# Kernel optimization log

Measured on AMD Instinct MI355X. Metric: run time of the kernel, lower is better.

Reference implementation:

```python
import jax, jax.numpy as jnp
import numpy as np

NUM_NODES = 100000
NUM_EDGES = 2500000
NUM_GRAPHS = 512
NODE_DIM = 7
STATE_DIM = 32
M = 2
ROUNDS = 4


def setup_inputs() -> dict:
    key = jax.random.key(0)
    ks = jax.random.split(key, 16)
    x = jax.random.normal(ks[0], (NUM_NODES, NODE_DIM), dtype=jnp.float32)
    edge_index = jax.random.randint(ks[1], (2, NUM_EDGES), 0, NUM_NODES)
    batch = jnp.sort(jax.random.randint(ks[2], (NUM_NODES,), 0, NUM_GRAPHS))
    s = 1.0 / np.sqrt(STATE_DIM)
    W_in = jax.random.normal(ks[3], (NODE_DIM, STATE_DIM), dtype=jnp.float32) / np.sqrt(NODE_DIM)
    b_in = jnp.zeros((STATE_DIM,), dtype=jnp.float32)
    W_msg = jax.random.normal(ks[4], (ROUNDS, STATE_DIM, STATE_DIM), dtype=jnp.float32) * s
    b_msg = jnp.zeros((ROUNDS, STATE_DIM), dtype=jnp.float32)
    W_upd = jax.random.normal(ks[5], (ROUNDS, STATE_DIM, STATE_DIM), dtype=jnp.float32) * s
    b_upd = jnp.zeros((ROUNDS, STATE_DIM), dtype=jnp.float32)
    W_out = jax.random.normal(ks[6], (STATE_DIM, 2 * M), dtype=jnp.float32) * s
    b_out = jnp.zeros((2 * M,), dtype=jnp.float32)
    return {"x": x, "edge_index": edge_index, "batch": batch,
            "W_in": W_in, "b_in": b_in, "W_msg": W_msg, "b_msg": b_msg,
            "W_upd": W_upd, "b_upd": b_upd, "W_out": W_out, "b_out": b_out}


def reference(x, edge_index, batch, W_in, b_in, W_msg, b_msg, W_upd, b_upd, W_out, b_out):
    # input net
    state = jax.nn.relu(x @ W_in + b_in)  # (N, S)
    src, dst = edge_index[0], edge_index[1]
    for r in range(ROUNDS):
        message = jax.nn.relu(state @ W_msg[r] + b_msg[r])          # (N, S)
        gathered = message[src]                                      # (E, S) irregular gather
        aggregated = jax.ops.segment_sum(gathered, dst, num_segments=NUM_NODES)  # scatter-add
        state = state + jax.nn.relu(aggregated @ W_upd[r] + b_upd[r])
    graph_state = jax.ops.segment_sum(state, batch, num_segments=NUM_GRAPHS)     # (G, S)
    out = graph_state @ W_out + b_out                                # (G, 2M)
    mean, log_std = jnp.split(out, 2, axis=-1)
    # Gaussian head: return mean and std (scale = exp(log_std)) concatenated
    return jnp.concatenate([mean, jnp.exp(log_std)], axis=-1)
```

## Files before the change

### kernel.cpp

```cpp
#include <hip/hip_runtime.h>
#include <hip/hip_fp8.h>
#include <math.h>

#define N_NODES 100000
#define N_EDGES 2500000
#define N_GRAPHS 512
#define NODE_DIM 7
#define S 32
#define ROUNDS 4

#define BKT_SHIFT 8
#define BKT_NODES 256
#define NBKT ((N_NODES + BKT_NODES - 1) / BKT_NODES)
#define CAP 7168
#define NSLOT 64
#define SLOT_PAD 32
#define CUR_PAD 32

#define NBIN_BLOCKS 512
#define NBIN_THREADS 512
#define TILE ((N_EDGES + NBIN_BLOCKS - 1) / NBIN_BLOCKS)

#define GN (N_NODES * S / 256)
#define GG (N_NODES / 16)

__device__ __forceinline__ void block_max_publish(float v, float* slots, int bid, int tid) {
    __shared__ float wmax[4];
#pragma unroll
    for (int o = 32; o > 0; o >>= 1) v = fmaxf(v, __shfl_xor(v, o, 64));
    if ((tid & 63) == 0) wmax[tid >> 6] = v;
    __syncthreads();
    if (tid == 0) {
        float m = fmaxf(fmaxf(wmax[0], wmax[1]), fmaxf(wmax[2], wmax[3]));
        atomicMax((unsigned int*)&slots[(bid & (NSLOT - 1)) * SLOT_PAD], __float_as_uint(m));
    }
}

__device__ __forceinline__ void acc4_fp8(unsigned int u, float& a0, float& a1,
                                         float& a2, float& a3) {
#if __has_builtin(__builtin_amdgcn_cvt_pk_f32_fp8)
    typedef float v2f __attribute__((ext_vector_type(2)));
    v2f lo = __builtin_amdgcn_cvt_pk_f32_fp8((int)u, false);
    v2f hi = __builtin_amdgcn_cvt_pk_f32_fp8((int)u, true);
    a0 += lo.x; a1 += lo.y; a2 += hi.x; a3 += hi.y;
#else
    __hip_fp8_e4m3 t0, t1, t2, t3;
    t0.__x = u & 0xff; t1.__x = (u >> 8) & 0xff;
    t2.__x = (u >> 16) & 0xff; t3.__x = (u >> 24) & 0xff;
    a0 += (float)t0; a1 += (float)t1; a2 += (float)t2; a3 += (float)t3;
#endif
}

__global__ void k_input(const float* __restrict__ x, const float* __restrict__ W_in,
                        const float* __restrict__ b_in, float* __restrict__ state,
                        float* __restrict__ graph_state, int* __restrict__ cursor,
                        float* __restrict__ tmpmax) {
    __shared__ float sW[NODE_DIM * S];
    __shared__ float sb[S];
    __shared__ float wmax[4];
    int tid = threadIdx.x;
    if (tid < NODE_DIM * S) sW[tid] = W_in[tid];
    if (tid < S) sb[tid] = b_in[tid];
    __syncthreads();
    int gid = blockIdx.x * blockDim.x + tid;
    if (gid < N_GRAPHS * S) graph_state[gid] = 0.f;
    if (gid < NBKT * CUR_PAD) cursor[gid] = 0;
    int n = gid >> 5, j = gid & 31;
    float acc = sb[j];
#pragma unroll
    for (int k = 0; k < NODE_DIM; k++) acc += x[n * NODE_DIM + k] * sW[k * S + j];
    float v = fmaxf(acc, 0.f);
    state[gid] = v;
#pragma unroll
    for (int o = 32; o > 0; o >>= 1) v = fmaxf(v, __shfl_xor(v, o, 64));
    if ((tid & 63) == 0) wmax[tid >> 6] = v;
    __syncthreads();
    if (tid == 0)
        tmpmax[blockIdx.x] = fmaxf(fmaxf(wmax[0], wmax[1]), fmaxf(wmax[2], wmax[3]));
}

__global__ void k_bin(const int* __restrict__ src, const int* __restrict__ dst,
                      int* __restrict__ cursor, int* __restrict__ binned,
                      const float* __restrict__ tmpmax, float* __restrict__ smax0) {
    __shared__ int pval[TILE];
    __shared__ unsigned short bkt[TILE];
    __shared__ unsigned short sidx[TILE];
    __shared__ int cnt[NBKT];
    __shared__ int base[NBKT];
    __shared__ int gbase[NBKT];
    __shared__ int sm[NBIN_THREADS];
    __shared__ float red[8];
    int tid = threadIdx.x;
    if (blockIdx.x == 0) {
        float mx = 0.f;
        for (int i = tid; i < GN; i += NBIN_THREADS) mx = fmaxf(mx, tmpmax[i]);
#pragma unroll
        for (int o = 32; o > 0; o >>= 1) mx = fmaxf(mx, __shfl_xor(mx, o, 64));
        if ((tid & 63) == 0) red[tid >> 6] = mx;
        __syncthreads();
        if (tid == 0) {
            float g = 0.f;
#pragma unroll
            for (int k = 0; k < 8; k++) g = fmaxf(g, red[k]);
            smax0[0] = g;
        } else if (tid < NSLOT) {
            smax0[tid * SLOT_PAD] = 0.f;
        }
    }
    int b0 = blockIdx.x * TILE;
    int m = min(TILE, N_EDGES - b0);
    if (m < 0) m = 0;
    for (int k = tid; k < NBKT; k += NBIN_THREADS) cnt[k] = 0;
    __syncthreads();
    for (int i = tid; i < m; i += NBIN_THREADS) {
        int d = dst[b0 + i];
        int s = src[b0 + i];
        int k = d >> BKT_SHIFT;
        pval[i] = (s << BKT_SHIFT) | (d & (BKT_NODES - 1));
        bkt[i] = (unsigned short)k;
        atomicAdd(&cnt[k], 1);
    }
    __syncthreads();
    int v = (tid < NBKT) ? cnt[tid] : 0;
    sm[tid] = v;
    __syncthreads();
    for (int off = 1; off < NBIN_THREADS; off <<= 1) {
        int add = (tid >= off) ? sm[tid - off] : 0;
        __syncthreads();
        sm[tid] += add;
        __syncthreads();
    }
    if (tid < NBKT) {
        base[tid] = sm[tid] - v;
        gbase[tid] = v ? atomicAdd(&cursor[tid * CUR_PAD], v) : 0;
        cnt[tid] = 0;
    }
    __syncthreads();
    for (int i = tid; i < m; i += NBIN_THREADS) {
        int k = bkt[i];
        int r = atomicAdd(&cnt[k], 1);
        sidx[base[k] + r] = (unsigned short)i;
    }
    __syncthreads();
    for (int i = tid; i < m; i += NBIN_THREADS) {
        int e = sidx[i];
        int k = bkt[e];
        int lpos = gbase[k] + (i - base[k]);
        if (lpos < CAP)
            binned[(size_t)k * CAP + lpos] = pval[e];
    }
}

__global__ void k_fill2(const int* __restrict__ cursor, int* __restrict__ binned,
                        int* __restrict__ row_beg, int* __restrict__ row_end) {
    __shared__ int stage[CAP];
    __shared__ int cnt[BKT_NODES];
    __shared__ int sm[BKT_NODES];
    int tid = threadIdx.x;
    int bkt = blockIdx.x;
    int beg = bkt * CAP;
    int m = min(cursor[bkt * CUR_PAD], CAP);
    for (int i = tid; i < m; i += 256) stage[i] = binned[beg + i];
    cnt[tid] = 0;
    __syncthreads();
    for (int i = tid; i < m; i += 256) atomicAdd(&cnt[stage[i] & (BKT_NODES - 1)], 1);
    __syncthreads();
    int v = cnt[tid];
    sm[tid] = v;
    __syncthreads();
    for (int off = 1; off < BKT_NODES; off <<= 1) {
        int add = (tid >= off) ? sm[tid - off] : 0;
        __syncthreads();
        sm[tid] += add;
        __syncthreads();
    }
    {
        int excl = sm[tid] - v;
        cnt[tid] = excl;
        int n = bkt * BKT_NODES + tid;
        if (n < N_NODES) { row_beg[n] = beg + excl; row_end[n] = beg + excl + v; }
    }
    __syncthreads();
    for (int i = tid; i < m; i += 256) {
        int ent = stage[i];
        int p = atomicAdd(&cnt[ent & (BKT_NODES - 1)], 1);
        binned[beg + p] = ent >> BKT_SHIFT;
    }
}

__global__ void k_msg(const float* __restrict__ state, const float* __restrict__ W,
                      const float* __restrict__ b, const float* __restrict__ smax_slots,
                      float* __restrict__ smax_next, float* __restrict__ inv_scale_out,
                      __hip_fp8_e4m3* __restrict__ message) {
    __shared__ float sW[S * S];
    __shared__ float sb[S];
    __shared__ float ssc[S];
    int tid = threadIdx.x;
    if (blockIdx.x < NSLOT && tid == 0) smax_next[blockIdx.x * SLOT_PAD] = 0.f;
    for (int i = tid; i < S * S; i += 256) sW[i] = W[i];
    if (tid < S) sb[tid] = b[tid];
    __syncthreads();
    if (tid < S) {
        float smax = 0.f;
#pragma unroll
        for (int k = 0; k < NSLOT; k++) smax = fmaxf(smax, smax_slots[k * SLOT_PAD]);
        float cs = 0.f;
#pragma unroll
        for (int k = 0; k < S; k++) cs += fabsf(sW[k * S + tid]);
        float bound = smax * cs + fabsf(sb[tid]) + 1e-20f;
        int e = (int)floorf(log2f(400.f / bound));
        e = max(-60, min(60, e));
        ssc[tid] = exp2f((float)e);
        if (blockIdx.x == 0) inv_scale_out[tid] = exp2f((float)-e);
    }
    __syncthreads();
    int gid = blockIdx.x * 256 + tid;
    int j = tid & 31;
    float my = state[gid];
    float acc = sb[j];
#pragma unroll
    for (int k = 0; k < S; k++) acc += __shfl(my, k, 32) * sW[k * S + j];
    float m = fminf(fmaxf(acc, 0.f) * ssc[j], 440.f);
    message[gid] = __hip_fp8_e4m3(m);
}

__global__ void k_gather_upd(const int* __restrict__ row_beg, const int* __restrict__ row_end,
                             const int* __restrict__ csr_src,
                             const unsigned char* __restrict__ message,
                             const float* __restrict__ W, const float* __restrict__ b,
                             const float* __restrict__ inv_scale,
                             float* __restrict__ state, float* __restrict__ smax_next) {
    __shared__ float sW[S * S];
    __shared__ float sb[S];
    __shared__ float si[S];
    int tid = threadIdx.x;
    for (int i = tid; i < S * S; i += 256) sW[i] = W[i];
    if (tid < S) { sb[tid] = b[tid]; si[tid] = inv_scale[tid]; }
    __syncthreads();
    int g = tid >> 5, j = tid & 31;
    int n0 = blockIdx.x * 16 + g * 2;
    int n1 = n0 + 1;
    int es = j >> 3;
    int qd = j & 7;
    int b0 = row_beg[n0], e0 = row_end[n0];
    int b1 = row_beg[n1], e1 = row_end[n1];
    float a0 = 0.f, a1 = 0.f, a2 = 0.f, a3 = 0.f;
    float c0 = 0.f, c1 = 0.f, c2 = 0.f, c3 = 0.f;
    for (; b0 < e0 || b1 < e1; b0 += 32, b1 += 32) {
        int sid0 = (b0 + j < e0) ? csr_src[b0 + j] : 0;
        int sid1 = (b1 + j < e1) ? csr_src[b1 + j] : 0;
        unsigned int u0[8], u1[8];
#pragma unroll
        for (int p = 0; p < 8; p++) {
            int s = __shfl(sid0, p * 4 + es, 32);
            unsigned int* ap = (unsigned int*)(message + (unsigned)s * 32u + (unsigned)qd * 4u);
            u0[p] = __hip_atomic_load(ap, __ATOMIC_RELAXED, __HIP_MEMORY_SCOPE_AGENT);
        }
#pragma unroll
        for (int p = 0; p < 8; p++) {
            int s = __shfl(sid1, p * 4 + es, 32);
            unsigned int* ap = (unsigned int*)(message + (unsigned)s * 32u + (unsigned)qd * 4u);
            u1[p] = __hip_atomic_load(ap, __ATOMIC_RELAXED, __HIP_MEMORY_SCOPE_AGENT);
        }
#pragma unroll
        for (int p = 0; p < 8; p++) {
            unsigned int uv = (b0 + p * 4 + es < e0) ? u0[p] : 0u;
            acc4_fp8(uv, a0, a1, a2, a3);
        }
#pragma unroll
        for (int p = 0; p < 8; p++) {
            unsigned int uv = (b1 + p * 4 + es < e1) ? u1[p] : 0u;
            acc4_fp8(uv, c0, c1, c2, c3);
        }
    }
    a0 += __shfl_xor(a0, 8, 32); a0 += __shfl_xor(a0, 16, 32);
    a1 += __shfl_xor(a1, 8, 32); a1 += __shfl_xor(a1, 16, 32);
    a2 += __shfl_xor(a2, 8, 32); a2 += __shfl_xor(a2, 16, 32);
    a3 += __shfl_xor(a3, 8, 32); a3 += __shfl_xor(a3, 16, 32);
    c0 += __shfl_xor(c0, 8, 32); c0 += __shfl_xor(c0, 16, 32);
    c1 += __shfl_xor(c1, 8, 32); c1 += __shfl_xor(c1, 16, 32);
    c2 += __shfl_xor(c2, 8, 32); c2 += __shfl_xor(c2, 16, 32);
    c3 += __shfl_xor(c3, 8, 32); c3 += __shfl_xor(c3, 16, 32);
    float s0 = si[4 * qd + 0], s1 = si[4 * qd + 1];
    float s2 = si[4 * qd + 2], s3 = si[4 * qd + 3];
    a0 *= s0; a1 *= s1; a2 *= s2; a3 *= s3;
    c0 *= s0; c1 *= s1; c2 *= s2; c3 *= s3;
    float u0v = sb[j], u1v = sb[j];
#pragma unroll
    for (int k = 0; k < S; k++) {
        float av, cv;
        switch (k & 3) {
            case 0: av = __shfl(a0, k >> 2, 32); cv = __shfl(c0, k >> 2, 32); break;
            case 1: av = __shfl(a1, k >> 2, 32); cv = __shfl(c1, k >> 2, 32); break;
            case 2: av = __shfl(a2, k >> 2, 32); cv = __shfl(c2, k >> 2, 32); break;
            default: av = __shfl(a3, k >> 2, 32); cv = __shfl(c3, k >> 2, 32); break;
        }
        float w = sW[k * S + j];
        u0v += av * w;
        u1v += cv * w;
    }
    size_t i0 = (size_t)n0 * S + j, i1 = (size_t)n1 * S + j;
    float ns0 = state[i0] + fmaxf(u0v, 0.f);
    float ns1 = state[i1] + fmaxf(u1v, 0.f);
    state[i0] = ns0;
    state[i1] = ns1;
    block_max_publish(fmaxf(ns0, ns1), smax_next, blockIdx.x, tid);
}

__global__ void k_pool(const float* __restrict__ state, const int* __restrict__ batch,
                       float* __restrict__ graph_state) {
    const int CHUNK = 32;
    const int nchunks = (N_NODES + CHUNK - 1) / CHUNK;
    int gid = blockIdx.x * blockDim.x + threadIdx.x;
    if (gid >= nchunks * S) return;
    int c = gid >> 5, j = gid & 31;
    int n0 = c * CHUNK;
    int n1 = min(n0 + CHUNK, N_NODES);
    float acc = 0.f;
    int curb = batch[n0];
    for (int n = n0; n < n1; n++) {
        int bn = batch[n];
        if (bn != curb) {
            atomicAdd(&graph_state[curb * S + j], acc);
            acc = 0.f;
            curb = bn;
        }
        acc += state[(size_t)n * S + j];
    }
    atomicAdd(&graph_state[curb * S + j], acc);
}

__global__ void k_head(const float* __restrict__ graph_state, const float* __restrict__ W_out,
                       const float* __restrict__ b_out, float* __restrict__ out) {
    int gid = blockIdx.x * blockDim.x + threadIdx.x;
    if (gid >= N_GRAPHS * 4) return;
    int g = gid >> 2, j = gid & 3;
    float acc = b_out[j];
#pragma unroll
    for (int k = 0; k < S; k++) acc += graph_state[g * S + k] * W_out[k * 4 + j];
    out[gid] = (j < 2) ? acc : expf(fminf(acc, 88.0f));
}

extern "C" void kernel_launch(void* const* d_in, const int* in_sizes, int n_in,
                              void* d_out, int out_size, void* d_ws, size_t ws_size,
                              hipStream_t stream) {
    const float* x     = (const float*)d_in[0];
    const int*   ei    = (const int*)d_in[1];
    const int*   batch = (const int*)d_in[2];
    const float* W_in  = (const float*)d_in[3];
    const float* b_in  = (const float*)d_in[4];
    const float* W_msg = (const float*)d_in[5];
    const float* b_msg = (const float*)d_in[6];
    const float* W_upd = (const float*)d_in[7];
    const float* b_upd = (const float*)d_in[8];
    const float* W_out = (const float*)d_in[9];
    const float* b_out = (const float*)d_in[10];
    float* out = (float*)d_out;

    float* state            = (float*)d_ws;
    __hip_fp8_e4m3* message = (__hip_fp8_e4m3*)(state + (size_t)N_NODES * S);
    float* graph_state      = (float*)((char*)message + (size_t)N_NODES * S);
    float* smax             = graph_state + N_GRAPHS * S;
    float* inv_scale        = smax + (ROUNDS + 1) * NSLOT * SLOT_PAD;
    float* tmpmax           = inv_scale + S;
    int*   row_beg          = (int*)(tmpmax + GN);
    int*   row_end          = row_beg + N_NODES;
    int*   cursor           = row_end + N_NODES;
    int*   binned           = cursor + NBKT * CUR_PAD;

    const int* src = ei;
    const int* dst = ei + N_EDGES;

    k_input<<<GN, dim3(256), 0, stream>>>(x, W_in, b_in, state, graph_state, cursor, tmpmax);
    k_bin<<<NBIN_BLOCKS, dim3(NBIN_THREADS), 0, stream>>>(src, dst, cursor, binned, tmpmax, smax);
    k_fill2<<<NBKT, dim3(256), 0, stream>>>(cursor, binned, row_beg, row_end);

    for (int r = 0; r < ROUNDS; r++) {
        k_msg<<<GN, dim3(256), 0, stream>>>(state, W_msg + r * S * S, b_msg + r * S,
                                            smax + r * NSLOT * SLOT_PAD,
                                            smax + (r + 1) * NSLOT * SLOT_PAD,
                                            inv_scale, message);
        k_gather_upd<<<GG, dim3(256), 0, stream>>>(row_beg, row_end, binned,
                                                   (const unsigned char*)message,
                                                   W_upd + r * S * S, b_upd + r * S,
                                                   inv_scale, state,
                                                   smax + (r + 1) * NSLOT * SLOT_PAD);
    }

    const int CHUNK = 32;
    int nchunks = (N_NODES + CHUNK - 1) / CHUNK;
    int gP = (nchunks * S + 255) / 256;
    k_pool<<<gP, dim3(256), 0, stream>>>(state, batch, graph_state);

    k_head<<<(N_GRAPHS * 4 + 255) / 256, dim3(256), 0, stream>>>(graph_state, W_out, b_out, out);
}
```

Before: 363.0 us.

## Fuse next-round message computation into gather-update kernel with a priori fp8 scale bound

Computes the next round's message (state @ W_msg + relu + fp8 quantization) inside the gather/update kernel, which removes three separate k_msg launches and one full re-read of state per round. Messages are double-buffered so the kernel can read round r while writing round r+1. Because the exact max of the new state is not known before the kernel runs, the fp8 scale is derived from a conservative upper bound built from the previous max, the max in-degree, the previous inv_scale and the update weights. That bound can be loose and may make the fp8 quantization coarser, and the extra shared memory and registers may lower occupancy of the gather kernel.

```diff
diff --git a/kernel.cpp b/kernel.cpp
--- a/kernel.cpp
+++ b/kernel.cpp
@@ -16,6 +16,7 @@
 #define NSLOT 64
 #define SLOT_PAD 32
 #define CUR_PAD 32
+#define NSP (NSLOT * SLOT_PAD)
 
 #define NBIN_BLOCKS 512
 #define NBIN_THREADS 512
@@ -54,7 +55,7 @@
 __global__ void k_input(const float* __restrict__ x, const float* __restrict__ W_in,
                         const float* __restrict__ b_in, float* __restrict__ state,
                         float* __restrict__ graph_state, int* __restrict__ cursor,
-                        float* __restrict__ tmpmax) {
+                        float* __restrict__ tmpmax, int* __restrict__ degmax) {
     __shared__ float sW[NODE_DIM * S];
     __shared__ float sb[S];
     __shared__ float wmax[4];
@@ -65,6 +66,7 @@
     int gid = blockIdx.x * blockDim.x + tid;
     if (gid < N_GRAPHS * S) graph_state[gid] = 0.f;
     if (gid < NBKT * CUR_PAD) cursor[gid] = 0;
+    if (gid == 0) *degmax = 0;
     int n = gid >> 5, j = gid & 31;
     float acc = sb[j];
 #pragma unroll
@@ -152,10 +154,12 @@
 }
 
 __global__ void k_fill2(const int* __restrict__ cursor, int* __restrict__ binned,
-                        int* __restrict__ row_beg, int* __restrict__ row_end) {
+                        int* __restrict__ row_beg, int* __restrict__ row_end,
+                        int* __restrict__ degmax) {
     __shared__ int stage[CAP];
     __shared__ int cnt[BKT_NODES];
     __shared__ int sm[BKT_NODES];
+    __shared__ int dmx[4];
     int tid = threadIdx.x;
     int bkt = blockIdx.x;
     int beg = bkt * CAP;
@@ -186,6 +190,12 @@
         int p = atomicAdd(&cnt[ent & (BKT_NODES - 1)], 1);
         binned[beg + p] = ent >> BKT_SHIFT;
     }
+    int dm = v;
+#pragma unroll
+    for (int o = 32; o > 0; o >>= 1) dm = max(dm, __shfl_xor(dm, o, 64));
+    if ((tid & 63) == 0) dmx[tid >> 6] = dm;
+    __syncthreads();
+    if (tid == 0) atomicMax(degmax, max(max(dmx[0], dmx[1]), max(dmx[2], dmx[3])));
 }
 
 __global__ void k_msg(const float* __restrict__ state, const float* __restrict__ W,
@@ -224,18 +234,57 @@
     message[gid] = __hip_fp8_e4m3(m);
 }
 
-__global__ void k_gather_upd(const int* __restrict__ row_beg, const int* __restrict__ row_end,
+__global__ void k_gather_msg(const int* __restrict__ row_beg, const int* __restrict__ row_end,
                              const int* __restrict__ csr_src,
-                             const unsigned char* __restrict__ message,
+                             const unsigned char* __restrict__ msg_in,
                              const float* __restrict__ W, const float* __restrict__ b,
-                             const float* __restrict__ inv_scale,
-                             float* __restrict__ state, float* __restrict__ smax_next) {
+                             const float* __restrict__ inv_scale_r,
+                             float* __restrict__ state,
+                             const float* __restrict__ smax_r,
+                             float* __restrict__ smax_next,
+                             float* __restrict__ smax_zero,
+                             const float* __restrict__ W_msg_next,
+                             const float* __restrict__ b_msg_next,
+                             const int* __restrict__ degmax_ptr,
+                             float* __restrict__ inv_scale_next,
+                             __hip_fp8_e4m3* __restrict__ msg_out)
+{
     __shared__ float sW[S * S];
+    __shared__ float sWm[S * S];
     __shared__ float sb[S];
     __shared__ float si[S];
+    __shared__ float sbm[S];
+    __shared__ float sscn[S];
     int tid = threadIdx.x;
+    if (smax_zero && blockIdx.x < NSLOT && tid == 0) smax_zero[blockIdx.x * SLOT_PAD] = 0.f;
     for (int i = tid; i < S * S; i += 256) sW[i] = W[i];
-    if (tid < S) { sb[tid] = b[tid]; si[tid] = inv_scale[tid]; }
+    if (tid < S) { sb[tid] = b[tid]; si[tid] = inv_scale_r[tid]; }
+    if (msg_out) {
+        for (int i = tid; i < S * S; i += 256) sWm[i] = W_msg_next[i];
+        if (tid < S) sbm[tid] = b_msg_next[tid];
+    }
+    __syncthreads();
+    if (msg_out && tid < S) {
+        float m = fmaxf(smax_r[tid * SLOT_PAD], smax_r[(tid + 32) * SLOT_PAD]);
+#pragma unroll
+        for (int o = 16; o > 0; o >>= 1) m = fmaxf(m, __shfl_xor(m, o, 32));
+        float dmax = (float)(*degmax_ptr);
+        float ub = 0.f;
+#pragma unroll
+        for (int k = 0; k < S; k++) ub += 440.f * si[k] * fabsf(sW[k * S + tid]);
+        ub = dmax * ub + fabsf(sb[tid]);
+#pragma unroll
+        for (int o = 16; o > 0; o >>= 1) ub = fmaxf(ub, __shfl_xor(ub, o, 32));
+        float mnext = m + ub;
+        float cs = 0.f;
+#pragma unroll
+        for (int k = 0; k < S; k++) cs += fabsf(sWm[k * S + tid]);
+        float bound = mnext * cs + fabsf(sbm[tid]) + 1e-20f;
+        int e = (int)floorf(log2f(400.f / bound));
+        e = max(-60, min(60, e));
+        sscn[tid] = exp2f((float)e);
+        if (blockIdx.x == 0) inv_scale_next[tid] = exp2f((float)-e);
+    }
     __syncthreads();
     int g = tid >> 5, j = tid & 31;
     int n0 = blockIdx.x * 16 + g * 2;
@@ -253,13 +302,13 @@
 #pragma unroll
         for (int p = 0; p < 8; p++) {
             int s = __shfl(sid0, p * 4 + es, 32);
-            unsigned int* ap = (unsigned int*)(message + (unsigned)s * 32u + (unsigned)qd * 4u);
+            unsigned int* ap = (unsigned int*)(msg_in + (unsigned)s * 32u + (unsigned)qd * 4u);
             u0[p] = __hip_atomic_load(ap, __ATOMIC_RELAXED, __HIP_MEMORY_SCOPE_AGENT);
         }
 #pragma unroll
         for (int p = 0; p < 8; p++) {
             int s = __shfl(sid1, p * 4 + es, 32);
-            unsigned int* ap = (unsigned int*)(message + (unsigned)s * 32u + (unsigned)qd * 4u);
+            unsigned int* ap = (unsigned int*)(msg_in + (unsigned)s * 32u + (unsigned)qd * 4u);
             u1[p] = __hip_atomic_load(ap, __ATOMIC_RELAXED, __HIP_MEMORY_SCOPE_AGENT);
         }
 #pragma unroll
@@ -304,6 +353,19 @@
     float ns1 = state[i1] + fmaxf(u1v, 0.f);
     state[i0] = ns0;
     state[i1] = ns1;
+    if (msg_out) {
+        float v0 = sbm[j], v1 = sbm[j];
+#pragma unroll
+        for (int k = 0; k < S; k++) {
+            float w = sWm[k * S + j];
+            v0 += __shfl(ns0, k, 32) * w;
+            v1 += __shfl(ns1, k, 32) * w;
+        }
+        float q0 = fminf(fmaxf(v0, 0.f) * sscn[j], 440.f);
+        float q1 = fminf(fmaxf(v1, 0.f) * sscn[j], 440.f);
+        msg_out[(size_t)n0 * S + j] = __hip_fp8_e4m3(q0);
+        msg_out[(size_t)n1 * S + j] = __hip_fp8_e4m3(q1);
+    }
     block_max_publish(fmaxf(ns0, ns1), smax_next, blockIdx.x, tid);
 }
 
@@ -358,33 +420,45 @@
     float* out = (float*)d_out;
 
     float* state            = (float*)d_ws;
-    __hip_fp8_e4m3* message = (__hip_fp8_e4m3*)(state + (size_t)N_NODES * S);
-    float* graph_state      = (float*)((char*)message + (size_t)N_NODES * S);
+    __hip_fp8_e4m3* msg0    = (__hip_fp8_e4m3*)(state + (size_t)N_NODES * S);
+    __hip_fp8_e4m3* msg1    = msg0 + (size_t)N_NODES * S;
+    float* graph_state      = (float*)(msg1 + (size_t)N_NODES * S);
     float* smax             = graph_state + N_GRAPHS * S;
-    float* inv_scale        = smax + (ROUNDS + 1) * NSLOT * SLOT_PAD;
-    float* tmpmax           = inv_scale + S;
+    float* inv_scale        = smax + (ROUNDS + 1) * NSP;
+    float* tmpmax           = inv_scale + ROUNDS * S;
     int*   row_beg          = (int*)(tmpmax + GN);
     int*   row_end          = row_beg + N_NODES;
     int*   cursor           = row_end + N_NODES;
-    int*   binned           = cursor + NBKT * CUR_PAD;
+    int*   degmax           = cursor + NBKT * CUR_PAD;
+    int*   binned           = degmax + 32;
 
     const int* src = ei;
     const int* dst = ei + N_EDGES;
 
-    k_input<<<GN, dim3(256), 0, stream>>>(x, W_in, b_in, state, graph_state, cursor, tmpmax);
-    k_bin<<<NBIN_BLOCKS, dim3(NBIN_THREADS), 0, stream>>>(src, dst, cursor, binned, tmpmax, smax);
-    k_fill2<<<NBKT, dim3(256), 0, stream>>>(cursor, binned, row_beg, row_end);
+    k_input<<<GN, dim3(256), 0, stream>>>(x, W_in, b_in, state, graph_state, cursor,
+                                          tmpmax, degmax);
+    k_bin<<<NBIN_BLOCKS, dim3(NBIN_THREADS), 0, stream>>>(src, dst, cursor, binned,
+                                                          tmpmax, smax);
+    k_fill2<<<NBKT, dim3(256), 0, stream>>>(cursor, binned, row_beg, row_end, degmax);
+    k_msg<<<GN, dim3(256), 0, stream>>>(state, W_msg, b_msg, smax, smax + NSP,
+                                        inv_scale, msg0);
 
     for (int r = 0; r < ROUNDS; r++) {
-        k_msg<<<GN, dim3(256), 0, stream>>>(state, W_msg + r * S * S, b_msg + r * S,
-                                            smax + r * NSLOT * SLOT_PAD,
-                                            smax + (r + 1) * NSLOT * SLOT_PAD,
-                                            inv_scale, message);
-        k_gather_upd<<<GG, dim3(256), 0, stream>>>(row_beg, row_end, binned,
-                                                   (const unsigned char*)message,
-                                                   W_upd + r * S * S, b_upd + r * S,
-                                                   inv_scale, state,
-                                                   smax + (r + 1) * NSLOT * SLOT_PAD);
+        const unsigned char* min_ = (const unsigned char*)((r & 1) ? msg1 : msg0);
+        __hip_fp8_e4m3* mout = (r < ROUNDS - 1) ? ((r & 1) ? msg0 : msg1) : nullptr;
+        k_gather_msg<<<GG, dim3(256), 0, stream>>>(
+            row_beg, row_end, binned, min_,
+            W_upd + r * S * S, b_upd + r * S,
+            inv_scale + r * S,
+            state,
+            smax + r * NSP,
+            smax + (r + 1) * NSP,
+            (r + 2 <= ROUNDS) ? smax + (r + 2) * NSP : nullptr,
+            (r < ROUNDS - 1) ? W_msg + (r + 1) * S * S : nullptr,
+            (r < ROUNDS - 1) ? b_msg + (r + 1) * S : nullptr,
+            degmax,
+            (r < ROUNDS - 1) ? inv_scale + (r + 1) * S : nullptr,
+            mout);
     }
 
     const int CHUNK = 32;
```

After: 342.3 us. -5.7%, faster.
